# Performance work log

Hardware: AMD Instinct MI355X
Metric: run time of the kernel (lower is better)

## Reference

```python
import jax, jax.numpy as jnp
import numpy as np

N_NODES = 100000


def gcn_conv(x, W, b, src, dst, n):
    """PyG GCNConv: add self-loops, symmetric normalization, aggregate."""
    x = x @ W  # [N, out]
    loop = jnp.arange(n, dtype=src.dtype)
    src_f = jnp.concatenate([src, loop])  # sources (message origins)
    dst_f = jnp.concatenate([dst, loop])  # targets (aggregation index)
    ones = jnp.ones(src_f.shape[0], dtype=x.dtype)
    deg = jax.ops.segment_sum(ones, dst_f, num_segments=n)
    dinv = jnp.where(deg > 0, jax.lax.rsqrt(deg), 0.0)
    norm = dinv[src_f] * dinv[dst_f]  # [E+N]
    msg = x[src_f] * norm[:, None]  # gather + scale
    out = jax.ops.segment_sum(msg, dst_f, num_segments=n)  # scatter-add
    return out + b


def setup_inputs() -> dict:
    key = jax.random.key(0)
    k1, k2, k3, k4 = jax.random.split(key, 4)
    in_f, hid, ncls = 128, 128, 64
    n_edges = 1600000
    x = jax.random.normal(k1, (N_NODES, in_f), dtype=jnp.float32)
    W1 = jax.random.normal(k2, (in_f, hid), dtype=jnp.float32) * (1.0 / np.sqrt(in_f))
    b1 = jnp.zeros((hid,), dtype=jnp.float32)
    W2 = jax.random.normal(k3, (hid, ncls), dtype=jnp.float32) * (1.0 / np.sqrt(hid))
    b2 = jnp.zeros((ncls,), dtype=jnp.float32)
    edge_index = jax.random.randint(k4, (2, n_edges), 0, N_NODES, dtype=jnp.int32)
    return {"x": x, "W1": W1, "b1": b1, "W2": W2, "b2": b2, "edge_index": edge_index}


def reference(x, W1, b1, W2, b2, edge_index):
    src, dst = edge_index[0], edge_index[1]
    n = x.shape[0]
    h = gcn_conv(x, W1, b1, src, dst, n)
    h = jax.nn.relu(h)
    # dropout p=0.5 is identity in eval mode
    h = gcn_conv(h, W2, b2, src, dst, n)
    return jax.nn.log_softmax(h, axis=1)
```

## Files before the change

### kernel.cpp

```cpp
#include <hip/hip_runtime.h>
#include <math.h>

#define N_NODES 100000
#define N_EDGES 1600000
#define NB 391
#define MROWS 100096
#define CH 3200
#define ZROW N_NODES

typedef __attribute__((ext_vector_type(8))) short short8;
typedef __attribute__((ext_vector_type(4))) float f32x4;
typedef __attribute__((ext_vector_type(2))) float f32x2;

__device__ __forceinline__ short f2b(float f) {
    unsigned u = __float_as_uint(f);
    unsigned r = (u + 0x7FFFu + ((u >> 16) & 1u)) >> 16;
    return (short)r;
}
__device__ __forceinline__ unsigned pk2(float a, float b) {
    return (unsigned)(unsigned short)f2b(a) | ((unsigned)(unsigned short)f2b(b) << 16);
}
__device__ __forceinline__ unsigned char f2q(float v) {
    return (unsigned char)(__builtin_amdgcn_cvt_pk_fp8_f32(v, 0.f, 0, false) & 0xFF);
}
__device__ __forceinline__ void acc4(float* a, unsigned u) {
    f32x2 lo = __builtin_amdgcn_cvt_pk_f32_fp8((int)u, false);
    f32x2 hi = __builtin_amdgcn_cvt_pk_f32_fp8((int)u, true);
    a[0] += lo[0]; a[1] += lo[1]; a[2] += hi[0]; a[3] += hi[1];
}

__device__ __forceinline__ short8 pack8t(const float* __restrict__ p) {
    float4 v0 = ((const float4*)p)[0];
    float4 v1 = ((const float4*)p)[1];
    union { unsigned u[4]; short8 s; } r;
    r.u[0] = __builtin_amdgcn_perm(__float_as_uint(v0.y), __float_as_uint(v0.x), 0x07060302u);
    r.u[1] = __builtin_amdgcn_perm(__float_as_uint(v0.w), __float_as_uint(v0.z), 0x07060302u);
    r.u[2] = __builtin_amdgcn_perm(__float_as_uint(v1.y), __float_as_uint(v1.x), 0x07060302u);
    r.u[3] = __builtin_amdgcn_perm(__float_as_uint(v1.w), __float_as_uint(v1.z), 0x07060302u);
    return r.s;
}

__global__ __launch_bounds__(256) void bucket_count(const int* __restrict__ dst,
                                                    int* __restrict__ bcnt) {
    __shared__ int h[NB];
    int t = threadIdx.x;
    for (int i = t; i < NB; i += 256) h[i] = 0;
    __syncthreads();
    for (int e = blockIdx.x * 256 + t; e < N_EDGES; e += gridDim.x * 256)
        atomicAdd(&h[dst[e] >> 8], 1);
    __syncthreads();
    for (int i = t; i < NB; i += 256)
        if (h[i]) atomicAdd(&bcnt[i], h[i]);
}

__global__ __launch_bounds__(512) void bucket_scan(const int* __restrict__ bcnt,
                                                   int* __restrict__ boffs,
                                                   int* __restrict__ bcur) {
    __shared__ int s[512];
    int t = threadIdx.x;
    int v = (t < NB) ? bcnt[t] : 0;
    s[t] = v;
    __syncthreads();
    for (int off = 1; off < 512; off <<= 1) {
        int u = (t >= off) ? s[t - off] : 0;
        __syncthreads();
        s[t] += u;
        __syncthreads();
    }
    if (t < NB) {
        int ex = s[t] - v;
        boffs[t] = ex;
        bcur[t] = ex;
    }
    if (t == 0) boffs[NB] = N_EDGES;
}

__global__ __launch_bounds__(256) void bucket_scatter(const int* __restrict__ src,
                                                      const int* __restrict__ dst,
                                                      int* __restrict__ bcur,
                                                      unsigned* __restrict__ pairs) {
    __shared__ unsigned lw[CH];
    __shared__ short lb[CH];
    __shared__ int cnt[NB];
    __shared__ int lstart[NB];
    int t = threadIdx.x;
    int e0 = blockIdx.x * CH;
    int n = min(CH, N_EDGES - e0);
    for (int i = t; i < NB; i += 256) cnt[i] = 0;
    __syncthreads();
    for (int i = t; i < n; i += 256) {
        int s = src[e0 + i], d = dst[e0 + i];
        lw[i] = ((unsigned)(d & 255) << 24) | (unsigned)s;
        int b = d >> 8;
        lb[i] = (short)b;
        atomicAdd(&cnt[b], 1);
    }
    __syncthreads();
    for (int b = t; b < NB; b += 256) {
        int c = cnt[b];
        lstart[b] = c ? atomicAdd(&bcur[b], c) : 0;
        cnt[b] = 0;
    }
    __syncthreads();
    for (int i = t; i < n; i += 256) {
        int b = lb[i];
        int lo = atomicAdd(&cnt[b], 1);
        pairs[lstart[b] + lo] = lw[i];
    }
}

__global__ __launch_bounds__(256) void csr_fill_bucket(const unsigned* __restrict__ pairs,
                                                       const int* __restrict__ boffs,
                                                       int2* __restrict__ rinfo,
                                                       float* __restrict__ dinv,
                                                       int* __restrict__ srcs) {
    __shared__ int lcnt[256];
    __shared__ int ls[256];
    int t = threadIdx.x, b = blockIdx.x, base = b << 8;
    lcnt[t] = 0;
    __syncthreads();
    int lo_e = boffs[b], hi_e = boffs[b + 1];
    for (int i = lo_e + t; i < hi_e; i += 256)
        atomicAdd(&lcnt[pairs[i] >> 24], 1);
    __syncthreads();
    int c = lcnt[t];
    int cpad = (c + 15) & ~15;
    ls[t] = cpad;
    __syncthreads();
    for (int off = 1; off < 256; off <<= 1) {
        int u = (t >= off) ? ls[t - off] : 0;
        __syncthreads();
        ls[t] += u;
        __syncthreads();
    }
    int pbase = ((lo_e + 15) & ~15) + b * 4096;
    int rp = pbase + ls[t] - cpad;
    int node = base + t;
    if (node < N_NODES) {
        rinfo[node] = make_int2(rp, rp + cpad);
        dinv[node] = rsqrtf((float)(c + 1));
    }
    __syncthreads();
    lcnt[t] = rp;
    __syncthreads();
    for (int i = lo_e + t; i < hi_e; i += 256) {
        unsigned p = pairs[i];
        int li = p >> 24;
        int pos = atomicAdd(&lcnt[li], 1);
        srcs[pos] = (int)(p & 0xFFFFFFu);
    }
    __syncthreads();
    for (int i = lcnt[t], stop = rp + cpad; i < stop; ++i) srcs[i] = ZROW;
}

__global__ __launch_bounds__(256) void convert_w(const float* __restrict__ W1,
                                                 const float* __restrict__ W2,
                                                 short* __restrict__ w1h,
                                                 short* __restrict__ w2h) {
    int id = blockIdx.x * 256 + threadIdx.x;
    if (id < 128 * 128) {
        int n = id >> 7, k = id & 127;
        w1h[id] = f2b(W1[k * 128 + n]);
    } else if (id < 128 * 128 + 64 * 128) {
        int j = id - 128 * 128;
        int n = j >> 7, k = j & 127;
        w2h[j] = f2b(W2[k * 64 + n]);
    }
}

__global__ __launch_bounds__(512) void gemm1_mfma(const float* __restrict__ X,
                                                  const short* __restrict__ Wt,
                                                  const float* __restrict__ dinv,
                                                  unsigned char* __restrict__ Yf) {
    __shared__ short Ws[128 * 128];
    const int t = threadIdx.x;
    for (int i = t * 8; i < 128 * 128; i += 512 * 8)
        *(short8*)(Ws + i) = *(const short8*)(Wt + i);
    __syncthreads();

    const int w = t >> 6, lane = t & 63;
    const int m = lane & 15, q = lane >> 4;
    const int r0 = blockIdx.x * 128 + w * 16;
    const int ra = min(r0 + m, N_NODES - 1);

    f32x4 acc[8];
#pragma unroll
    for (int c = 0; c < 8; ++c) acc[c] = (f32x4)(0.f);

#pragma unroll
    for (int kk = 0; kk < 4; ++kk) {
        const int koff = kk * 32 + q * 8;
        short8 a = pack8t(X + (size_t)ra * 128 + koff);
#pragma unroll
        for (int c = 0; c < 8; ++c) {
            short8 bh = *(const short8*)(Ws + (c * 16 + m) * 128 + koff);
            acc[c] = __builtin_amdgcn_mfma_f32_16x16x32_bf16(a, bh, acc[c], 0, 0, 0);
        }
    }

    const int rb0 = r0 + q * 4;
    f32x4 dv = *(const f32x4*)(dinv + rb0);
#pragma unroll
    for (int c = 0; c < 8; ++c) {
        const int col = c * 16 + m;
#pragma unroll
        for (int r = 0; r < 4; ++r) {
            int row = rb0 + r;
            if (row < N_NODES) Yf[(size_t)row * 128 + col] = f2q(acc[c][r] * dv[r]);
        }
    }
}

__global__ __launch_bounds__(512) void gemm2_mfma(const short* __restrict__ H,
                                                  const short* __restrict__ Wt,
                                                  const float* __restrict__ dinv,
                                                  unsigned char* __restrict__ Yf) {
    __shared__ short Ws[64 * 128];
    const int t = threadIdx.x;
    for (int i = t * 8; i < 64 * 128; i += 512 * 8)
        *(short8*)(Ws + i) = *(const short8*)(Wt + i);
    __syncthreads();

    const int w = t >> 6, lane = t & 63;
    const int m = lane & 15, q = lane >> 4;
    const int r0 = blockIdx.x * 128 + w * 16;

    f32x4 acc[4];
#pragma unroll
    for (int c = 0; c < 4; ++c) acc[c] = (f32x4)(0.f);

#pragma unroll
    for (int kk = 0; kk < 4; ++kk) {
        const int koff = kk * 32 + q * 8;
        short8 a = *(const short8*)(H + (size_t)(r0 + m) * 128 + koff);
#pragma unroll
        for (int c = 0; c < 4; ++c) {
            short8 bh = *(const short8*)(Ws + (c * 16 + m) * 128 + koff);
            acc[c] = __builtin_amdgcn_mfma_f32_16x16x32_bf16(a, bh, acc[c], 0, 0, 0);
        }
    }

    const int rb0 = r0 + q * 4;
    f32x4 dv = *(const f32x4*)(dinv + rb0);
#pragma unroll
    for (int c = 0; c < 4; ++c) {
        const int col = c * 16 + m;
#pragma unroll
        for (int r = 0; r < 4; ++r) {
            int row = rb0 + r;
            if (row < N_NODES) Yf[(size_t)row * 64 + col] = f2q(acc[c][r] * dv[r]);
        }
    }
}

__global__ __launch_bounds__(256) void agg_relu(const int2* __restrict__ rinfo,
                                                const int* __restrict__ srcs,
                                                const unsigned char* __restrict__ Yf,
                                                const float* __restrict__ dinv,
                                                const float* __restrict__ b,
                                                short* __restrict__ Hb) {
    int t = threadIdx.x;
    int lane = t & 63, w = t >> 6;
    int half = lane >> 5, li = lane & 31;
    int d = blockIdx.x * 4 + w;
    if (d >= N_NODES) return;
    const unsigned fo = (unsigned)(li << 2);
    int2 ri = rinfo[d];
    unsigned selfu = *(const unsigned*)(Yf + (((unsigned)d << 7) + fo));
    float a[4] = {0.f, 0.f, 0.f, 0.f};
    for (int e = ri.x; e < ri.y; e += 16) {
        const int* sp = srcs + e + 8 * half;
        uint4 s0 = *(const uint4*)sp;
        uint4 s1 = *(const uint4*)(sp + 4);
        unsigned g0 = *(const unsigned*)(Yf + (((unsigned)s0.x << 7) + fo));
        unsigned g1 = *(const unsigned*)(Yf + (((unsigned)s0.y << 7) + fo));
        unsigned g2 = *(const unsigned*)(Yf + (((unsigned)s0.z << 7) + fo));
        unsigned g3 = *(const unsigned*)(Yf + (((unsigned)s0.w << 7) + fo));
        unsigned g4 = *(const unsigned*)(Yf + (((unsigned)s1.x << 7) + fo));
        unsigned g5 = *(const unsigned*)(Yf + (((unsigned)s1.y << 7) + fo));
        unsigned g6 = *(const unsigned*)(Yf + (((unsigned)s1.z << 7) + fo));
        unsigned g7 = *(const unsigned*)(Yf + (((unsigned)s1.w << 7) + fo));
        acc4(a, g0); acc4(a, g1); acc4(a, g2); acc4(a, g3);
        acc4(a, g4); acc4(a, g5); acc4(a, g6); acc4(a, g7);
    }
    if (!half) acc4(a, selfu);
#pragma unroll
    for (int i = 0; i < 4; ++i) a[i] += __shfl_xor(a[i], 32);
    if (!half) {
        float sc = dinv[d];
        float4 bb = ((const float4*)b)[li];
        float v0 = fmaxf(sc * a[0] + bb.x, 0.f);
        float v1 = fmaxf(sc * a[1] + bb.y, 0.f);
        float v2 = fmaxf(sc * a[2] + bb.z, 0.f);
        float v3 = fmaxf(sc * a[3] + bb.w, 0.f);
        ((uint2*)Hb)[(size_t)d * 32 + li] = make_uint2(pk2(v0, v1), pk2(v2, v3));
    }
}

__global__ __launch_bounds__(256) void agg_lsm(const int2* __restrict__ rinfo,
                                               const int* __restrict__ srcs,
                                               const unsigned char* __restrict__ Yf,
                                               const float* __restrict__ dinv,
                                               const float* __restrict__ b,
                                               float* __restrict__ out) {
    int t = threadIdx.x;
    int lane = t & 63, w = t >> 6;
    int gi = lane >> 4, li = lane & 15;
    int d = blockIdx.x * 4 + w;
    if (d >= N_NODES) return;
    const unsigned fo = (unsigned)(li << 2);
    int2 ri = rinfo[d];
    unsigned selfu = *(const unsigned*)(Yf + (((unsigned)d << 6) + fo));
    float a[4] = {0.f, 0.f, 0.f, 0.f};
    for (int e = ri.x; e < ri.y; e += 16) {
        uint4 sv = *(const uint4*)(srcs + e + 4 * gi);
        unsigned g0 = *(const unsigned*)(Yf + (((unsigned)sv.x << 6) + fo));
        unsigned g1 = *(const unsigned*)(Yf + (((unsigned)sv.y << 6) + fo));
        unsigned g2 = *(const unsigned*)(Yf + (((unsigned)sv.z << 6) + fo));
        unsigned g3 = *(const unsigned*)(Yf + (((unsigned)sv.w << 6) + fo));
        acc4(a, g0); acc4(a, g1); acc4(a, g2); acc4(a, g3);
    }
    if (gi == 0) acc4(a, selfu);
#pragma unroll
    for (int i = 0; i < 4; ++i) {
        a[i] += __shfl_xor(a[i], 16);
        a[i] += __shfl_xor(a[i], 32);
    }
    float sc = dinv[d];
    float4 bb = ((const float4*)b)[li];
    float v0 = sc * a[0] + bb.x;
    float v1 = sc * a[1] + bb.y;
    float v2 = sc * a[2] + bb.z;
    float v3 = sc * a[3] + bb.w;
    float m = fmaxf(fmaxf(v0, v1), fmaxf(v2, v3));
#pragma unroll
    for (int o = 1; o <= 8; o <<= 1) m = fmaxf(m, __shfl_xor(m, o));
    float su = __expf(v0 - m) + __expf(v1 - m) + __expf(v2 - m) + __expf(v3 - m);
#pragma unroll
    for (int o = 1; o <= 8; o <<= 1) su += __shfl_xor(su, o);
    float ls = m + logf(su);
    if (gi == 0)
        ((float4*)out)[(size_t)d * 16 + li] =
            make_float4(v0 - ls, v1 - ls, v2 - ls, v3 - ls);
}

extern "C" void kernel_launch(void* const* d_in, const int* in_sizes, int n_in,
                              void* d_out, int out_size, void* d_ws, size_t ws_size,
                              hipStream_t stream) {
    const float* x  = (const float*)d_in[0];
    const float* W1 = (const float*)d_in[1];
    const float* b1 = (const float*)d_in[2];
    const float* W2 = (const float*)d_in[3];
    const float* b2 = (const float*)d_in[4];
    const int* edge = (const int*)d_in[5];
    const int* src = edge;
    const int* dst = edge + N_EDGES;
    float* out = (float*)d_out;

    char* ws = (char*)d_ws;
    int*           bcnt  = (int*)(ws + 0);
    int*           boffs = (int*)(ws + 2048);
    int*           bcur  = (int*)(ws + 4096);
    float*         dinv  = (float*)(ws + 6144);
    int2*          rinfo = (int2*)(ws + 406528);
    int*           srcs  = (int*)(ws + 1206528);
    unsigned*      pairs = (unsigned*)(ws + 14012672);
    short*         w1h   = (short*)(ws + 20412672);
    short*         w2h   = (short*)(ws + 20445440);
    unsigned char* y1f   = (unsigned char*)(ws + 20461824);
    short*         h1b   = (short*)(ws + 33274112);
    unsigned char* y2f   = (unsigned char*)(ws + 58898688);

    hipMemsetAsync(y1f + (size_t)N_NODES * 128, 0, 128, stream);
    hipMemsetAsync(y2f + (size_t)N_NODES * 64, 0, 64, stream);

    hipMemsetAsync(bcnt, 0, NB * sizeof(int), stream);
    bucket_count<<<512, 256, 0, stream>>>(dst, bcnt);
    bucket_scan<<<1, 512, 0, stream>>>(bcnt, boffs, bcur);
    bucket_scatter<<<(N_EDGES + CH - 1) / CH, 256, 0, stream>>>(src, dst, bcur, pairs);
    csr_fill_bucket<<<NB, 256, 0, stream>>>(pairs, boffs, rinfo, dinv, srcs);

    convert_w<<<(128 * 128 + 64 * 128 + 255) / 256, 256, 0, stream>>>(W1, W2, w1h, w2h);

    gemm1_mfma<<<MROWS / 128, 512, 0, stream>>>(x, w1h, dinv, y1f);
    agg_relu<<<(N_NODES + 3) / 4, 256, 0, stream>>>(rinfo, srcs, y1f, dinv, b1, h1b);

    gemm2_mfma<<<MROWS / 128, 512, 0, stream>>>(h1b, w2h, dinv, y2f);
    agg_lsm<<<(N_NODES + 3) / 4, 256, 0, stream>>>(rinfo, srcs, y2f, dinv, b2, out);
}
```

Baseline: 271.8 us.

## Process two nodes per wavefront in aggregation and pad CSR rows to 8

The aggregation kernels now give each wavefront two destination nodes and interleave their edge loops, so gathers from two rows are in flight at once. CSR row padding drops from 16 to 8, which cuts wasted zero-row gathers, and the per-bucket slack region shrinks to match. The three memsets are replaced by one small init kernel to reduce launch overhead. The two-node loop adds divergence when the two degrees differ, and it assumes N_NODES is a multiple of 8.

```diff
diff --git a/kernel.cpp b/kernel.cpp
--- a/kernel.cpp
+++ b/kernel.cpp
@@ -40,6 +40,15 @@
     return r.s;
 }
 
+__global__ __launch_bounds__(512) void init_misc(int* __restrict__ bcnt,
+                                                 unsigned* __restrict__ y1s,
+                                                 unsigned* __restrict__ y2s) {
+    int t = threadIdx.x;
+    if (t < NB) bcnt[t] = 0;
+    if (t < 32) y1s[t] = 0;
+    if (t < 16) y2s[t] = 0;
+}
+
 __global__ __launch_bounds__(256) void bucket_count(const int* __restrict__ dst,
                                                     int* __restrict__ bcnt) {
     __shared__ int h[NB];
@@ -124,7 +133,7 @@
         atomicAdd(&lcnt[pairs[i] >> 24], 1);
     __syncthreads();
     int c = lcnt[t];
-    int cpad = (c + 15) & ~15;
+    int cpad = (c + 7) & ~7;
     ls[t] = cpad;
     __syncthreads();
     for (int off = 1; off < 256; off <<= 1) {
@@ -133,7 +142,7 @@
         ls[t] += u;
         __syncthreads();
     }
-    int pbase = ((lo_e + 15) & ~15) + b * 4096;
+    int pbase = ((lo_e + 7) & ~7) + b * 2048;
     int rp = pbase + ls[t] - cpad;
     int node = base + t;
     if (node < N_NODES) {
@@ -262,39 +271,57 @@
     int t = threadIdx.x;
     int lane = t & 63, w = t >> 6;
     int half = lane >> 5, li = lane & 31;
-    int d = blockIdx.x * 4 + w;
-    if (d >= N_NODES) return;
+    int d0 = blockIdx.x * 8 + 2 * w;
+    int d1 = d0 + 1;
     const unsigned fo = (unsigned)(li << 2);
-    int2 ri = rinfo[d];
-    unsigned selfu = *(const unsigned*)(Yf + (((unsigned)d << 7) + fo));
-    float a[4] = {0.f, 0.f, 0.f, 0.f};
-    for (int e = ri.x; e < ri.y; e += 16) {
-        const int* sp = srcs + e + 8 * half;
-        uint4 s0 = *(const uint4*)sp;
-        uint4 s1 = *(const uint4*)(sp + 4);
-        unsigned g0 = *(const unsigned*)(Yf + (((unsigned)s0.x << 7) + fo));
-        unsigned g1 = *(const unsigned*)(Yf + (((unsigned)s0.y << 7) + fo));
-        unsigned g2 = *(const unsigned*)(Yf + (((unsigned)s0.z << 7) + fo));
-        unsigned g3 = *(const unsigned*)(Yf + (((unsigned)s0.w << 7) + fo));
-        unsigned g4 = *(const unsigned*)(Yf + (((unsigned)s1.x << 7) + fo));
-        unsigned g5 = *(const unsigned*)(Yf + (((unsigned)s1.y << 7) + fo));
-        unsigned g6 = *(const unsigned*)(Yf + (((unsigned)s1.z << 7) + fo));
-        unsigned g7 = *(const unsigned*)(Yf + (((unsigned)s1.w << 7) + fo));
-        acc4(a, g0); acc4(a, g1); acc4(a, g2); acc4(a, g3);
-        acc4(a, g4); acc4(a, g5); acc4(a, g6); acc4(a, g7);
-    }
-    if (!half) acc4(a, selfu);
-#pragma unroll
-    for (int i = 0; i < 4; ++i) a[i] += __shfl_xor(a[i], 32);
-    if (!half) {
-        float sc = dinv[d];
-        float4 bb = ((const float4*)b)[li];
-        float v0 = fmaxf(sc * a[0] + bb.x, 0.f);
-        float v1 = fmaxf(sc * a[1] + bb.y, 0.f);
-        float v2 = fmaxf(sc * a[2] + bb.z, 0.f);
-        float v3 = fmaxf(sc * a[3] + bb.w, 0.f);
-        ((uint2*)Hb)[(size_t)d * 32 + li] = make_uint2(pk2(v0, v1), pk2(v2, v3));
-    }
+    int2 r0 = rinfo[d0], r1 = rinfo[d1];
+    float a0[4] = {0.f, 0.f, 0.f, 0.f};
+    float a1[4] = {0.f, 0.f, 0.f, 0.f};
+    {
+        unsigned dh = half ? (unsigned)d1 : (unsigned)d0;
+        unsigned su = *(const unsigned*)(Yf + ((dh << 7) + fo));
+        if (!half) acc4(a0, su); else acc4(a1, su);
+    }
+    int e0 = r0.x, n0 = r0.y, e1 = r1.x, n1 = r1.y;
+    while (true) {
+        bool c0 = e0 < n0, c1 = e1 < n1;
+        if (!(c0 | c1)) break;
+        if (c0) {
+            uint4 s = *(const uint4*)(srcs + e0 + 4 * half);
+            unsigned g0 = *(const unsigned*)(Yf + (((unsigned)s.x << 7) + fo));
+            unsigned g1 = *(const unsigned*)(Yf + (((unsigned)s.y << 7) + fo));
+            unsigned g2 = *(const unsigned*)(Yf + (((unsigned)s.z << 7) + fo));
+            unsigned g3 = *(const unsigned*)(Yf + (((unsigned)s.w << 7) + fo));
+            acc4(a0, g0); acc4(a0, g1); acc4(a0, g2); acc4(a0, g3);
+            e0 += 8;
+        }
+        if (c1) {
+            uint4 s = *(const uint4*)(srcs + e1 + 4 * half);
+            unsigned g0 = *(const unsigned*)(Yf + (((unsigned)s.x << 7) + fo));
+            unsigned g1 = *(const unsigned*)(Yf + (((unsigned)s.y << 7) + fo));
+            unsigned g2 = *(const unsigned*)(Yf + (((unsigned)s.z << 7) + fo));
+            unsigned g3 = *(const unsigned*)(Yf + (((unsigned)s.w << 7) + fo));
+            acc4(a1, g0); acc4(a1, g1); acc4(a1, g2); acc4(a1, g3);
+            e1 += 8;
+        }
+    }
+#pragma unroll
+    for (int i = 0; i < 4; ++i) {
+        a0[i] += __shfl_xor(a0[i], 32);
+        a1[i] += __shfl_xor(a1[i], 32);
+    }
+    int dd = half ? d1 : d0;
+    float s0 = half ? a1[0] : a0[0];
+    float s1 = half ? a1[1] : a0[1];
+    float s2 = half ? a1[2] : a0[2];
+    float s3 = half ? a1[3] : a0[3];
+    float sc = dinv[dd];
+    float4 bb = ((const float4*)b)[li];
+    float v0 = fmaxf(sc * s0 + bb.x, 0.f);
+    float v1 = fmaxf(sc * s1 + bb.y, 0.f);
+    float v2 = fmaxf(sc * s2 + bb.z, 0.f);
+    float v3 = fmaxf(sc * s3 + bb.w, 0.f);
+    ((uint2*)Hb)[(size_t)dd * 32 + li] = make_uint2(pk2(v0, v1), pk2(v2, v3));
 }
 
 __global__ __launch_bounds__(256) void agg_lsm(const int2* __restrict__ rinfo,
@@ -306,32 +333,56 @@
     int t = threadIdx.x;
     int lane = t & 63, w = t >> 6;
     int gi = lane >> 4, li = lane & 15;
-    int d = blockIdx.x * 4 + w;
-    if (d >= N_NODES) return;
+    int d0 = blockIdx.x * 8 + 2 * w;
+    int d1 = d0 + 1;
     const unsigned fo = (unsigned)(li << 2);
-    int2 ri = rinfo[d];
-    unsigned selfu = *(const unsigned*)(Yf + (((unsigned)d << 6) + fo));
-    float a[4] = {0.f, 0.f, 0.f, 0.f};
-    for (int e = ri.x; e < ri.y; e += 16) {
-        uint4 sv = *(const uint4*)(srcs + e + 4 * gi);
-        unsigned g0 = *(const unsigned*)(Yf + (((unsigned)sv.x << 6) + fo));
-        unsigned g1 = *(const unsigned*)(Yf + (((unsigned)sv.y << 6) + fo));
-        unsigned g2 = *(const unsigned*)(Yf + (((unsigned)sv.z << 6) + fo));
-        unsigned g3 = *(const unsigned*)(Yf + (((unsigned)sv.w << 6) + fo));
-        acc4(a, g0); acc4(a, g1); acc4(a, g2); acc4(a, g3);
-    }
-    if (gi == 0) acc4(a, selfu);
+    int2 r0 = rinfo[d0], r1 = rinfo[d1];
+    float a0[4] = {0.f, 0.f, 0.f, 0.f};
+    float a1[4] = {0.f, 0.f, 0.f, 0.f};
+    {
+        unsigned dh = (gi == 1) ? (unsigned)d1 : (unsigned)d0;
+        unsigned su = *(const unsigned*)(Yf + ((dh << 6) + fo));
+        if (gi == 0) acc4(a0, su);
+        else if (gi == 1) acc4(a1, su);
+    }
+    int e0 = r0.x, n0 = r0.y, e1 = r1.x, n1 = r1.y;
+    while (true) {
+        bool c0 = e0 < n0, c1 = e1 < n1;
+        if (!(c0 | c1)) break;
+        if (c0) {
+            uint2 s = *(const uint2*)(srcs + e0 + 2 * gi);
+            unsigned g0 = *(const unsigned*)(Yf + (((unsigned)s.x << 6) + fo));
+            unsigned g1 = *(const unsigned*)(Yf + (((unsigned)s.y << 6) + fo));
+            acc4(a0, g0); acc4(a0, g1);
+            e0 += 8;
+        }
+        if (c1) {
+            uint2 s = *(const uint2*)(srcs + e1 + 2 * gi);
+            unsigned g0 = *(const unsigned*)(Yf + (((unsigned)s.x << 6) + fo));
+            unsigned g1 = *(const unsigned*)(Yf + (((unsigned)s.y << 6) + fo));
+            acc4(a1, g0); acc4(a1, g1);
+            e1 += 8;
+        }
+    }
 #pragma unroll
     for (int i = 0; i < 4; ++i) {
-        a[i] += __shfl_xor(a[i], 16);
-        a[i] += __shfl_xor(a[i], 32);
-    }
-    float sc = dinv[d];
+        a0[i] += __shfl_xor(a0[i], 16);
+        a0[i] += __shfl_xor(a0[i], 32);
+        a1[i] += __shfl_xor(a1[i], 16);
+        a1[i] += __shfl_xor(a1[i], 32);
+    }
+    int gsel = gi >> 1;
+    int dd = gsel ? d1 : d0;
+    float s0 = gsel ? a1[0] : a0[0];
+    float s1 = gsel ? a1[1] : a0[1];
+    float s2 = gsel ? a1[2] : a0[2];
+    float s3 = gsel ? a1[3] : a0[3];
+    float sc = dinv[dd];
     float4 bb = ((const float4*)b)[li];
-    float v0 = sc * a[0] + bb.x;
-    float v1 = sc * a[1] + bb.y;
-    float v2 = sc * a[2] + bb.z;
-    float v3 = sc * a[3] + bb.w;
+    float v0 = sc * s0 + bb.x;
+    float v1 = sc * s1 + bb.y;
+    float v2 = sc * s2 + bb.z;
+    float v3 = sc * s3 + bb.w;
     float m = fmaxf(fmaxf(v0, v1), fmaxf(v2, v3));
 #pragma unroll
     for (int o = 1; o <= 8; o <<= 1) m = fmaxf(m, __shfl_xor(m, o));
@@ -339,8 +390,8 @@
 #pragma unroll
     for (int o = 1; o <= 8; o <<= 1) su += __shfl_xor(su, o);
     float ls = m + logf(su);
-    if (gi == 0)
-        ((float4*)out)[(size_t)d * 16 + li] =
+    if ((gi & 1) == 0)
+        ((float4*)out)[(size_t)dd * 16 + li] =
             make_float4(v0 - ls, v1 - ls, v2 - ls, v3 - ls);
 }
 
@@ -371,10 +422,10 @@
     short*         h1b   = (short*)(ws + 33274112);
     unsigned char* y2f   = (unsigned char*)(ws + 58898688);
 
-    hipMemsetAsync(y1f + (size_t)N_NODES * 128, 0, 128, stream);
-    hipMemsetAsync(y2f + (size_t)N_NODES * 64, 0, 64, stream);
-
-    hipMemsetAsync(bcnt, 0, NB * sizeof(int), stream);
+    init_misc<<<1, 512, 0, stream>>>(bcnt,
+                                     (unsigned*)(y1f + (size_t)N_NODES * 128),
+                                     (unsigned*)(y2f + (size_t)N_NODES * 64));
+
     bucket_count<<<512, 256, 0, stream>>>(dst, bcnt);
     bucket_scan<<<1, 512, 0, stream>>>(bcnt, boffs, bcur);
     bucket_scatter<<<(N_EDGES + CH - 1) / CH, 256, 0, stream>>>(src, dst, bcur, pairs);
@@ -383,8 +434,8 @@
     convert_w<<<(128 * 128 + 64 * 128 + 255) / 256, 256, 0, stream>>>(W1, W2, w1h, w2h);
 
     gemm1_mfma<<<MROWS / 128, 512, 0, stream>>>(x, w1h, dinv, y1f);
-    agg_relu<<<(N_NODES + 3) / 4, 256, 0, stream>>>(rinfo, srcs, y1f, dinv, b1, h1b);
+    agg_relu<<<N_NODES / 8, 256, 0, stream>>>(rinfo, srcs, y1f, dinv, b1, h1b);
 
     gemm2_mfma<<<MROWS / 128, 512, 0, stream>>>(h1b, w2h, dinv, y2f);
-    agg_lsm<<<(N_NODES + 3) / 4, 256, 0, stream>>>(rinfo, srcs, y2f, dinv, b2, out);
-}
+    agg_lsm<<<N_NODES / 8, 256, 0, stream>>>(rinfo, srcs, y2f, dinv, b2, out);
+}
```

Measured after the change: 268.5 us. No clear change (-1.2%).
